# Kernel tuning notes

Measured on AMD Instinct MI355X. Metric: run time of the kernel, lower is better.

The kernel has to match this reference:

```python
import jax, jax.numpy as jnp
import numpy as np
import math

C = 128
N_HEAD = 4
GROUPS = 16
EPS = 1e-5


def group_norm(x, w, b):
    # x: [B, C, H, W], normalize per group over (C//G, H, W)
    B, Ch, H, W = x.shape
    xg = x.reshape(B, GROUPS, Ch // GROUPS, H, W)
    mu = xg.mean(axis=(2, 3, 4), keepdims=True)
    var = xg.var(axis=(2, 3, 4), keepdims=True)
    xn = (xg - mu) * jax.lax.rsqrt(var + EPS)
    xn = xn.reshape(B, Ch, H, W)
    return xn * w[None, :, None, None] + b[None, :, None, None]


def conv1x1(x, w, b=None):
    # w: [out, in]; x: [B, in, H, W]
    y = jnp.einsum('oc,bchw->bohw', w, x)
    if b is not None:
        y = y + b[None, :, None, None]
    return y


def cross_attn(q, k, v):
    # q, k, v: [B, C, H, W] -> split heads, flatten spatial
    B, Ch, H, W = q.shape
    d = Ch // N_HEAD
    L = H * W
    qh = q.reshape(B, N_HEAD, d, L)
    kh = k.reshape(B, N_HEAD, d, L)
    vh = v.reshape(B, N_HEAD, d, L)
    # scale by sqrt(channel) as in the original (not sqrt(head_dim))
    scores = jnp.einsum('bndq,bndk->bnqk', qh, kh) / math.sqrt(Ch)
    attn = jax.nn.softmax(scores, axis=-1)
    out = jnp.einsum('bnqk,bndk->bndq', attn, vh)
    return out.reshape(B, Ch, H, W)


def setup_inputs() -> dict:
    key = jax.random.key(0)
    ks = jax.random.split(key, 8)
    B, H, W = 2, 64, 64
    inp = {
        'x_A': jax.random.normal(ks[0], (B, C, H, W), jnp.float32),
        'x_B': jax.random.normal(ks[1], (B, C, H, W), jnp.float32),
        'gn_w_A': jnp.ones((C,), jnp.float32),
        'gn_b_A': jnp.zeros((C,), jnp.float32),
        'gn_w_B': jnp.ones((C,), jnp.float32),
        'gn_b_B': jnp.zeros((C,), jnp.float32),
        'w_qkv_A': jax.random.normal(ks[2], (3 * C, C), jnp.float32) / math.sqrt(C),
        'w_qkv_B': jax.random.normal(ks[3], (3 * C, C), jnp.float32) / math.sqrt(C),
        'w_out_A': jax.random.normal(ks[4], (C, C), jnp.float32) / math.sqrt(C),
        'b_out_A': jnp.zeros((C,), jnp.float32),
        'w_out_B': jax.random.normal(ks[5], (C, C), jnp.float32) / math.sqrt(C),
        'b_out_B': jnp.zeros((C,), jnp.float32),
    }
    return inp


def reference(x_A, x_B, gn_w_A, gn_b_A, gn_w_B, gn_b_B,
              w_qkv_A, w_qkv_B, w_out_A, b_out_A, w_out_B, b_out_B):
    xA = group_norm(x_A, gn_w_A, gn_b_A)
    xB = group_norm(x_B, gn_w_B, gn_b_B)
    qkvA = conv1x1(xA, w_qkv_A)  # [B, 3C, H, W]
    qkvB = conv1x1(xB, w_qkv_B)
    # torch view(b, n_head, head_dim*3, h, w).chunk(3, dim=2) splits within each head
    B, _, H, W = xA.shape
    d = C // N_HEAD
    qkvA = qkvA.reshape(B, N_HEAD, 3, d, H, W)
    qkvB = qkvB.reshape(B, N_HEAD, 3, d, H, W)
    qA, kA, vA = [qkvA[:, :, i].reshape(B, C, H, W) for i in range(3)]
    qB, kB, vB = [qkvB[:, :, i].reshape(B, C, H, W) for i in range(3)]
    # out_A: queries from B attend to keys/values of A; residual on normalized xA
    attn_out_A = cross_attn(qB, kA, vA)
    out_A = conv1x1(attn_out_A, w_out_A, b_out_A) + xA
    attn_out_B = cross_attn(qA, kB, vB)
    out_B = conv1x1(attn_out_B, w_out_B, b_out_B) + xB
    return (out_A, out_B)
```

## Files before the change

### kernel.cpp

```cpp
#include <hip/hip_runtime.h>
#include <hip/hip_bf16.h>

typedef __attribute__((ext_vector_type(8))) short short8;
typedef __attribute__((ext_vector_type(4))) short s16x4;
typedef __attribute__((ext_vector_type(4))) float f32x4;
typedef __attribute__((ext_vector_type(4))) float float4v;

#define L 4096
#define CCH 128
#define NH 4
#define HD 32
#define NSB 4
#define WQ_ELEMS 49152
#define WO_ELEMS 16384

static __device__ __forceinline__ unsigned short f2bf(float f) {
  unsigned int u = __float_as_uint(f);
  u += 0x7FFFu + ((u >> 16) & 1u);
  return (unsigned short)(u >> 16);
}

#if __has_builtin(__builtin_amdgcn_mfma_f32_16x16x16bf16_1k)
static __device__ __forceinline__ f32x4 mfma16(s16x4 a, s16x4 b, f32x4 c) {
  return __builtin_amdgcn_mfma_f32_16x16x16bf16_1k(a, b, c, 0, 0, 0);
}
#else
static __device__ __forceinline__ f32x4 mfma16(s16x4 a, s16x4 b, f32x4 c) {
  asm("v_mfma_f32_16x16x16_bf16 %0, %1, %2, %0"
      : "+v"(c) : "v"(a), "v"(b));
  return c;
}
#endif

__global__ void __launch_bounds__(256) wconv_kernel(
    const float* __restrict__ wqA, const float* __restrict__ wqB,
    const float* __restrict__ woA, const float* __restrict__ woB,
    unsigned short* __restrict__ wq, unsigned short* __restrict__ wo) {
  int i = (blockIdx.x * 256 + threadIdx.x) * 4;
  const float* src;
  unsigned short* dst;
  if (i < WQ_ELEMS)            { src = wqA + i;                     dst = wq + i; }
  else if (i < 2 * WQ_ELEMS)   { src = wqB + (i - WQ_ELEMS);        dst = wq + i; }
  else if (i < 2 * WQ_ELEMS + WO_ELEMS)
                               { src = woA + (i - 2 * WQ_ELEMS);    dst = wo + (i - 2 * WQ_ELEMS); }
  else                         { src = woB + (i - 2 * WQ_ELEMS - WO_ELEMS);
                                 dst = wo + (i - 2 * WQ_ELEMS); }
  float4v v = *(const float4v*)src;
  s16x4 o;
  #pragma unroll
  for (int j = 0; j < 4; ++j) o[j] = (short)f2bf(v[j]);
  *(s16x4*)dst = o;
}

__global__ void __launch_bounds__(256) gn_stats_kernel(
    const float* __restrict__ xA, const float* __restrict__ xB,
    float* __restrict__ stats) {
  int bid = blockIdx.x;
  int g = bid & 15;
  int b = (bid >> 4) & 1;
  int s = bid >> 5;
  const float* x = s ? xB : xA;
  const float* xb = x + (size_t)b * CCH * L + (size_t)g * 8 * L;
  int t = threadIdx.x;
  float sum = 0.f, sq = 0.f;
  for (int e = t * 4; e < 8 * L; e += 1024) {
    float4v v = *(const float4v*)(xb + e);
    #pragma unroll
    for (int j = 0; j < 4; ++j) { sum += v[j]; sq += v[j] * v[j]; }
  }
  #pragma unroll
  for (int off = 32; off; off >>= 1) {
    sum += __shfl_down(sum, off);
    sq  += __shfl_down(sq, off);
  }
  __shared__ float red[2][4];
  int w = t >> 6, lane = t & 63;
  if (lane == 0) { red[0][w] = sum; red[1][w] = sq; }
  __syncthreads();
  if (t == 0) {
    float S = red[0][0] + red[0][1] + red[0][2] + red[0][3];
    float Q = red[1][0] + red[1][1] + red[1][2] + red[1][3];
    float mu = S * (1.f / 32768.f);
    float var = Q * (1.f / 32768.f) - mu * mu;
    stats[bid * 2] = mu;
    stats[bid * 2 + 1] = rsqrtf(var + 1e-5f);
  }
}

__global__ void __launch_bounds__(256) gn_apply_kernel(
    const float* __restrict__ xA, const float* __restrict__ xB,
    const float* __restrict__ gwA, const float* __restrict__ gbA,
    const float* __restrict__ gwB, const float* __restrict__ gbB,
    const float* __restrict__ stats,
    float* __restrict__ xn, unsigned short* __restrict__ xnT) {
  int i = (blockIdx.x * 256 + threadIdx.x) * 8;
  int l = i & (L - 1);
  int c = (i >> 12) & 127;
  int sb = i >> 19;
  int s = sb >> 1, b = sb & 1, g = c >> 3;
  const float* x  = s ? xB : xA;
  const float* gw = s ? gwB : gwA;
  const float* gb = s ? gbB : gbA;
  float mu = stats[(sb * 16 + g) * 2];
  float rs = stats[(sb * 16 + g) * 2 + 1];
  float sc = rs * gw[c];
  float bi = gb[c] - mu * sc;
  const float* xp = x + (size_t)b * CCH * L + (size_t)c * L + l;
  float4v v0 = *(const float4v*)(xp);
  float4v v1 = *(const float4v*)(xp + 4);
  float r[8];
  #pragma unroll
  for (int j = 0; j < 4; ++j) { r[j] = v0[j] * sc + bi; r[4 + j] = v1[j] * sc + bi; }
  float* xo = xn + ((size_t)sb * CCH + c) * L + l;
  *(float4v*)(xo) = *(const float4v*)(r);
  *(float4v*)(xo + 4) = *(const float4v*)(r + 4);
  unsigned short* xt = xnT + ((size_t)sb * L + l) * CCH + c;
  #pragma unroll
  for (int j = 0; j < 8; ++j) xt[(size_t)j * CCH] = f2bf(r[j]);
}

__global__ void __launch_bounds__(256, 4) qkv_kernel(
    const unsigned short* __restrict__ wqbf,
    const unsigned short* __restrict__ xnT,
    unsigned short* __restrict__ qT, unsigned short* __restrict__ kT,
    unsigned short* __restrict__ vv) {
  int bid = blockIdx.x;
  int nc = bid & 63;
  int mt = (bid >> 6) % 24;
  int sb = bid / (24 * 64);
  int s = sb >> 1;
  const unsigned short* wq = wqbf + (size_t)s * WQ_ELEMS;
  int t = threadIdx.x;
  int w = t >> 6, lane = t & 63, ln = lane & 15, sub = lane >> 4;
  int obase = mt * 16;
  int lbase = nc * 64 + w * 16;
  const unsigned short* bbase = xnT + ((size_t)sb * L + lbase + ln) * CCH;
  const unsigned short* abase = wq + (size_t)(obase + ln) * CCH;
  f32x4 acc = {0.f, 0.f, 0.f, 0.f};
  #pragma unroll
  for (int kc = 0; kc < 4; ++kc) {
    int k0 = kc * 32 + sub * 8;
    short8 af = *(const short8*)(abase + k0);
    short8 bfr = *(const short8*)(bbase + k0);
    acc = __builtin_amdgcn_mfma_f32_16x16x32_bf16(af, bfr, acc, 0, 0, 0);
  }
  const float qscale = 0.08838834764831845f;
  int lcol = lbase + ln;
  #pragma unroll
  for (int r = 0; r < 4; ++r) {
    int o = obase + sub * 4 + r;
    int head = o / 96;
    int rem = o - head * 96;
    int part = rem >> 5;
    int dd = rem & 31;
    size_t bh = (size_t)sb * NH + head;
    if (part == 0)      qT[(bh * L + lcol) * HD + dd] = f2bf(acc[r] * qscale);
    else if (part == 1) kT[(bh * L + lcol) * HD + dd] = f2bf(acc[r]);
    else                vv[(bh * HD + dd) * L + lcol] = f2bf(acc[r]);
  }
}

__global__ void __launch_bounds__(256, 2) flash_kernel(
    const unsigned short* __restrict__ qT, const unsigned short* __restrict__ kT,
    const unsigned short* __restrict__ vv, unsigned short* __restrict__ ao) {
  int bid = blockIdx.x;
  int qt = bid & 31;
  int h  = (bid >> 5) & 3;
  int b  = (bid >> 7) & 1;
  int s  = bid >> 8;
  size_t bh_kv = (size_t)((s * 2 + b) * NH + h);
  size_t bh_q  = (size_t)(((s ^ 1) * 2 + b) * NH + h);
  const unsigned short* qTb = qT + bh_q * L * HD;
  const unsigned short* kTb = kT + bh_kv * L * HD;
  const unsigned short* vb  = vv + bh_kv * HD * L;

  int t = threadIdx.x;
  int w = t >> 6, lane = t & 63, ln = lane & 15, sub = lane >> 4;
  int qbase = qt * 128 + w * 32;

  short8 bq0 = *(const short8*)(qTb + (size_t)(qbase + ln) * HD + sub * 8);
  short8 bq1 = *(const short8*)(qTb + (size_t)(qbase + 16 + ln) * HD + sub * 8);

  f32x4 acc00 = {0.f, 0.f, 0.f, 0.f}, acc01 = {0.f, 0.f, 0.f, 0.f};
  f32x4 acc10 = {0.f, 0.f, 0.f, 0.f}, acc11 = {0.f, 0.f, 0.f, 0.f};
  float m0 = -1e30f, l0 = 0.f;
  float m1 = -1e30f, l1 = 0.f;

  for (int kt = 0; kt < L / 64; ++kt) {
    int kbase = kt * 64;
    short8 ak0 = *(const short8*)(kTb + (size_t)(kbase +  0 + ln) * HD + sub * 8);
    short8 ak1 = *(const short8*)(kTb + (size_t)(kbase + 16 + ln) * HD + sub * 8);
    short8 ak2 = *(const short8*)(kTb + (size_t)(kbase + 32 + ln) * HD + sub * 8);
    short8 ak3 = *(const short8*)(kTb + (size_t)(kbase + 48 + ln) * HD + sub * 8);
    s16x4 av00 = *(const s16x4*)(vb + (size_t)ln * L + kbase +  0 + sub * 4);
    s16x4 av01 = *(const s16x4*)(vb + (size_t)(16 + ln) * L + kbase +  0 + sub * 4);
    s16x4 av10 = *(const s16x4*)(vb + (size_t)ln * L + kbase + 16 + sub * 4);
    s16x4 av11 = *(const s16x4*)(vb + (size_t)(16 + ln) * L + kbase + 16 + sub * 4);
    s16x4 av20 = *(const s16x4*)(vb + (size_t)ln * L + kbase + 32 + sub * 4);
    s16x4 av21 = *(const s16x4*)(vb + (size_t)(16 + ln) * L + kbase + 32 + sub * 4);
    s16x4 av30 = *(const s16x4*)(vb + (size_t)ln * L + kbase + 48 + sub * 4);
    s16x4 av31 = *(const s16x4*)(vb + (size_t)(16 + ln) * L + kbase + 48 + sub * 4);

    f32x4 zz = {0.f, 0.f, 0.f, 0.f};
    f32x4 sa0 = __builtin_amdgcn_mfma_f32_16x16x32_bf16(ak0, bq0, zz, 0, 0, 0);
    f32x4 sa1 = __builtin_amdgcn_mfma_f32_16x16x32_bf16(ak1, bq0, zz, 0, 0, 0);
    f32x4 sa2 = __builtin_amdgcn_mfma_f32_16x16x32_bf16(ak2, bq0, zz, 0, 0, 0);
    f32x4 sa3 = __builtin_amdgcn_mfma_f32_16x16x32_bf16(ak3, bq0, zz, 0, 0, 0);
    f32x4 sb0 = __builtin_amdgcn_mfma_f32_16x16x32_bf16(ak0, bq1, zz, 0, 0, 0);
    f32x4 sb1 = __builtin_amdgcn_mfma_f32_16x16x32_bf16(ak1, bq1, zz, 0, 0, 0);
    f32x4 sb2 = __builtin_amdgcn_mfma_f32_16x16x32_bf16(ak2, bq1, zz, 0, 0, 0);
    f32x4 sb3 = __builtin_amdgcn_mfma_f32_16x16x32_bf16(ak3, bq1, zz, 0, 0, 0);

    s16x4 bp00, bp01, bp02, bp03;
    {
      float mx = fmaxf(fmaxf(sa0[0], sa0[1]), fmaxf(sa0[2], sa0[3]));
      mx = fmaxf(mx, fmaxf(fmaxf(sa1[0], sa1[1]), fmaxf(sa1[2], sa1[3])));
      mx = fmaxf(mx, fmaxf(fmaxf(sa2[0], sa2[1]), fmaxf(sa2[2], sa2[3])));
      mx = fmaxf(mx, fmaxf(fmaxf(sa3[0], sa3[1]), fmaxf(sa3[2], sa3[3])));
      mx = fmaxf(mx, __shfl_xor(mx, 16));
      mx = fmaxf(mx, __shfl_xor(mx, 32));
      float newm = fmaxf(m0, mx);
      float alpha = __expf(m0 - newm);
      float rsum = 0.f;
      #pragma unroll
      for (int r = 0; r < 4; ++r) {
        float p0 = __expf(sa0[r] - newm);
        float p1 = __expf(sa1[r] - newm);
        float p2 = __expf(sa2[r] - newm);
        float p3 = __expf(sa3[r] - newm);
        rsum += (p0 + p1) + (p2 + p3);
        bp00[r] = (short)f2bf(p0);
        bp01[r] = (short)f2bf(p1);
        bp02[r] = (short)f2bf(p2);
        bp03[r] = (short)f2bf(p3);
      }
      rsum += __shfl_xor(rsum, 16);
      rsum += __shfl_xor(rsum, 32);
      l0 = l0 * alpha + rsum;
      m0 = newm;
      #pragma unroll
      for (int r = 0; r < 4; ++r) { acc00[r] *= alpha; acc01[r] *= alpha; }
    }
    s16x4 bp10, bp11, bp12, bp13;
    {
      float mx = fmaxf(fmaxf(sb0[0], sb0[1]), fmaxf(sb0[2], sb0[3]));
      mx = fmaxf(mx, fmaxf(fmaxf(sb1[0], sb1[1]), fmaxf(sb1[2], sb1[3])));
      mx = fmaxf(mx, fmaxf(fmaxf(sb2[0], sb2[1]), fmaxf(sb2[2], sb2[3])));
      mx = fmaxf(mx, fmaxf(fmaxf(sb3[0], sb3[1]), fmaxf(sb3[2], sb3[3])));
      mx = fmaxf(mx, __shfl_xor(mx, 16));
      mx = fmaxf(mx, __shfl_xor(mx, 32));
      float newm = fmaxf(m1, mx);
      float alpha = __expf(m1 - newm);
      float rsum = 0.f;
      #pragma unroll
      for (int r = 0; r < 4; ++r) {
        float p0 = __expf(sb0[r] - newm);
        float p1 = __expf(sb1[r] - newm);
        float p2 = __expf(sb2[r] - newm);
        float p3 = __expf(sb3[r] - newm);
        rsum += (p0 + p1) + (p2 + p3);
        bp10[r] = (short)f2bf(p0);
        bp11[r] = (short)f2bf(p1);
        bp12[r] = (short)f2bf(p2);
        bp13[r] = (short)f2bf(p3);
      }
      rsum += __shfl_xor(rsum, 16);
      rsum += __shfl_xor(rsum, 32);
      l1 = l1 * alpha + rsum;
      m1 = newm;
      #pragma unroll
      for (int r = 0; r < 4; ++r) { acc10[r] *= alpha; acc11[r] *= alpha; }
    }
    acc00 = mfma16(av00, bp00, acc00); acc01 = mfma16(av01, bp00, acc01);
    acc00 = mfma16(av10, bp01, acc00); acc01 = mfma16(av11, bp01, acc01);
    acc00 = mfma16(av20, bp02, acc00); acc01 = mfma16(av21, bp02, acc01);
    acc00 = mfma16(av30, bp03, acc00); acc01 = mfma16(av31, bp03, acc01);
    acc10 = mfma16(av00, bp10, acc10); acc11 = mfma16(av01, bp10, acc11);
    acc10 = mfma16(av10, bp11, acc10); acc11 = mfma16(av11, bp11, acc11);
    acc10 = mfma16(av20, bp12, acc10); acc11 = mfma16(av21, bp12, acc11);
    acc10 = mfma16(av30, bp13, acc10); acc11 = mfma16(av31, bp13, acc11);
  }

  {
    float inv = 1.0f / l0;
    int qrow = qbase + ln;
    size_t rowoff = ((size_t)(s * 2 + b) * L + qrow) * CCH + h * HD;
    s16x4 o0, o1;
    #pragma unroll
    for (int r = 0; r < 4; ++r) {
      o0[r] = (short)f2bf(acc00[r] * inv);
      o1[r] = (short)f2bf(acc01[r] * inv);
    }
    *(s16x4*)(ao + rowoff + sub * 4) = o0;
    *(s16x4*)(ao + rowoff + 16 + sub * 4) = o1;
  }
  {
    float inv = 1.0f / l1;
    int qrow = qbase + 16 + ln;
    size_t rowoff = ((size_t)(s * 2 + b) * L + qrow) * CCH + h * HD;
    s16x4 o0, o1;
    #pragma unroll
    for (int r = 0; r < 4; ++r) {
      o0[r] = (short)f2bf(acc10[r] * inv);
      o1[r] = (short)f2bf(acc11[r] * inv);
    }
    *(s16x4*)(ao + rowoff + sub * 4) = o0;
    *(s16x4*)(ao + rowoff + 16 + sub * 4) = o1;
  }
}

__global__ void __launch_bounds__(256, 4) outproj_kernel(
    const unsigned short* __restrict__ wobf,
    const float* __restrict__ boA, const float* __restrict__ boB,
    const unsigned short* __restrict__ ao, const float* __restrict__ xn,
    float* __restrict__ out) {
  int bid = blockIdx.x;
  int nc = bid & 63;
  int mt = (bid >> 6) & 7;
  int sb = bid >> 9;
  int s = sb >> 1;
  int b = sb & 1;
  const unsigned short* wo = wobf + (size_t)s * WO_ELEMS;
  const float* bo = s ? boB : boA;
  int t = threadIdx.x;
  int w = t >> 6, lane = t & 63, ln = lane & 15, sub = lane >> 4;
  int obase = mt * 16;
  int lbase = nc * 64 + w * 16;
  const unsigned short* bbase = ao + ((size_t)sb * L + lbase + ln) * CCH;
  const unsigned short* abase = wo + (size_t)(obase + ln) * CCH;
  f32x4 acc = {0.f, 0.f, 0.f, 0.f};
  #pragma unroll
  for (int kc = 0; kc < 4; ++kc) {
    int k0 = kc * 32 + sub * 8;
    short8 af = *(const short8*)(abase + k0);
    short8 bfr = *(const short8*)(bbase + k0);
    acc = __builtin_amdgcn_mfma_f32_16x16x32_bf16(af, bfr, acc, 0, 0, 0);
  }
  int lcol = lbase + ln;
  #pragma unroll
  for (int r = 0; r < 4; ++r) {
    int o = obase + sub * 4 + r;
    out[(size_t)s * (2 * CCH * L) + ((size_t)b * CCH + o) * L + lcol] =
        acc[r] + bo[o] + xn[((size_t)sb * CCH + o) * L + lcol];
  }
}

extern "C" void kernel_launch(void* const* d_in, const int* in_sizes, int n_in,
                              void* d_out, int out_size, void* d_ws, size_t ws_size,
                              hipStream_t stream) {
  (void)in_sizes; (void)n_in; (void)out_size; (void)ws_size;
  const float* xA  = (const float*)d_in[0];
  const float* xB  = (const float*)d_in[1];
  const float* gwA = (const float*)d_in[2];
  const float* gbA = (const float*)d_in[3];
  const float* gwB = (const float*)d_in[4];
  const float* gbB = (const float*)d_in[5];
  const float* wqA = (const float*)d_in[6];
  const float* wqB = (const float*)d_in[7];
  const float* woA = (const float*)d_in[8];
  const float* boA = (const float*)d_in[9];
  const float* woB = (const float*)d_in[10];
  const float* boB = (const float*)d_in[11];
  float* out = (float*)d_out;

  char* ws = (char*)d_ws;
  size_t off = 0;
  float* xn = (float*)(ws + off);            off += (size_t)NSB * CCH * L * sizeof(float);
  unsigned short* xnT = (unsigned short*)(ws + off); off += (size_t)NSB * L * CCH * 2;
  unsigned short* qT  = (unsigned short*)(ws + off); off += (size_t)NSB * NH * L * HD * 2;
  unsigned short* kT  = (unsigned short*)(ws + off); off += (size_t)NSB * NH * L * HD * 2;
  unsigned short* vv  = (unsigned short*)(ws + off); off += (size_t)NSB * NH * HD * L * 2;
  unsigned short* ao  = (unsigned short*)(ws + off); off += (size_t)NSB * L * CCH * 2;
  float* stats = (float*)(ws + off);         off += 64 * 2 * sizeof(float);
  unsigned short* wqbf = (unsigned short*)(ws + off); off += (size_t)2 * WQ_ELEMS * 2;
  unsigned short* wobf = (unsigned short*)(ws + off); off += (size_t)2 * WO_ELEMS * 2;

  wconv_kernel<<<dim3(128), dim3(256), 0, stream>>>(wqA, wqB, woA, woB, wqbf, wobf);
  gn_stats_kernel<<<dim3(64), dim3(256), 0, stream>>>(xA, xB, stats);
  gn_apply_kernel<<<dim3(1024), dim3(256), 0, stream>>>(xA, xB, gwA, gbA, gwB, gbB,
                                                        stats, xn, xnT);
  qkv_kernel<<<dim3(NSB * 24 * 64), dim3(256), 0, stream>>>(wqbf, xnT, qT, kT, vv);
  flash_kernel<<<dim3(512), dim3(256), 0, stream>>>(qT, kT, vv, ao);
  outproj_kernel<<<dim3(NSB * 8 * 64), dim3(256), 0, stream>>>(wobf, boA, boB, ao, xn, out);
}
```

Baseline: 287.7 us.

## Stage K/V tiles through double-buffered LDS and remap block order in flash kernel

Each flash block previously had every wave load its own K and V fragments straight from global memory. Now the block loads each 64-key K/V tile once, cooperatively, into a double-buffered LDS area in MFMA fragment order. The global load for the next tile is issued before computing on the current one, so load latency overlaps compute. Block IDs are also permuted so consecutive blocks map to different heads and batches, which spreads L2 use. The cost is one __syncthreads per tile, extra LDS traffic and 16 KB of LDS per block, which may limit occupancy.

```diff
diff --git a/kernel.cpp b/kernel.cpp
--- a/kernel.cpp
+++ b/kernel.cpp
@@ -163,7 +163,8 @@
 __global__ void __launch_bounds__(256, 2) flash_kernel(
     const unsigned short* __restrict__ qT, const unsigned short* __restrict__ kT,
     const unsigned short* __restrict__ vv, unsigned short* __restrict__ ao) {
-  int bid = blockIdx.x;
+  int bid0 = blockIdx.x;
+  int bid = (bid0 & 7) * 64 + (bid0 >> 3);
   int qt = bid & 31;
   int h  = (bid >> 5) & 3;
   int b  = (bid >> 7) & 1;
@@ -178,29 +179,49 @@
   int w = t >> 6, lane = t & 63, ln = lane & 15, sub = lane >> 4;
   int qbase = qt * 128 + w * 32;
 
+  __shared__ unsigned short lds_k[2][2048];
+  __shared__ unsigned short lds_v[2][2048];
+
+  const unsigned short* gK = kTb + (size_t)(w * 16 + (lane >> 2)) * HD + (lane & 3) * 8;
+  int dstK = ((w * 4 + (lane & 3)) * 16 + (lane >> 2)) * 8;
+  int dV = w * 8 + (lane >> 3);
+  const unsigned short* gV = vb + (size_t)dV * L + (lane & 7) * 8;
+  int ttv = (lane & 7) >> 1, halfv = w >> 1, lnv = (w & 1) * 8 + (lane >> 3);
+  int sub0 = ((lane & 7) & 1) * 2;
+  int dstV0 = (((ttv * 2 + halfv) * 4 + sub0) * 16 + lnv) * 4;
+
   short8 bq0 = *(const short8*)(qTb + (size_t)(qbase + ln) * HD + sub * 8);
   short8 bq1 = *(const short8*)(qTb + (size_t)(qbase + 16 + ln) * HD + sub * 8);
+
+  {
+    short8 sk = *(const short8*)(gK);
+    short8 sv = *(const short8*)(gV);
+    s16x4 svlo, svhi;
+    #pragma unroll
+    for (int j = 0; j < 4; ++j) { svlo[j] = sv[j]; svhi[j] = sv[4 + j]; }
+    *(short8*)&lds_k[0][dstK] = sk;
+    *(s16x4*)&lds_v[0][dstV0] = svlo;
+    *(s16x4*)&lds_v[0][dstV0 + 64] = svhi;
+  }
+  __syncthreads();
 
   f32x4 acc00 = {0.f, 0.f, 0.f, 0.f}, acc01 = {0.f, 0.f, 0.f, 0.f};
   f32x4 acc10 = {0.f, 0.f, 0.f, 0.f}, acc11 = {0.f, 0.f, 0.f, 0.f};
   float m0 = -1e30f, l0 = 0.f;
   float m1 = -1e30f, l1 = 0.f;
 
-  for (int kt = 0; kt < L / 64; ++kt) {
-    int kbase = kt * 64;
-    short8 ak0 = *(const short8*)(kTb + (size_t)(kbase +  0 + ln) * HD + sub * 8);
-    short8 ak1 = *(const short8*)(kTb + (size_t)(kbase + 16 + ln) * HD + sub * 8);
-    short8 ak2 = *(const short8*)(kTb + (size_t)(kbase + 32 + ln) * HD + sub * 8);
-    short8 ak3 = *(const short8*)(kTb + (size_t)(kbase + 48 + ln) * HD + sub * 8);
-    s16x4 av00 = *(const s16x4*)(vb + (size_t)ln * L + kbase +  0 + sub * 4);
-    s16x4 av01 = *(const s16x4*)(vb + (size_t)(16 + ln) * L + kbase +  0 + sub * 4);
-    s16x4 av10 = *(const s16x4*)(vb + (size_t)ln * L + kbase + 16 + sub * 4);
-    s16x4 av11 = *(const s16x4*)(vb + (size_t)(16 + ln) * L + kbase + 16 + sub * 4);
-    s16x4 av20 = *(const s16x4*)(vb + (size_t)ln * L + kbase + 32 + sub * 4);
-    s16x4 av21 = *(const s16x4*)(vb + (size_t)(16 + ln) * L + kbase + 32 + sub * 4);
-    s16x4 av30 = *(const s16x4*)(vb + (size_t)ln * L + kbase + 48 + sub * 4);
-    s16x4 av31 = *(const s16x4*)(vb + (size_t)(16 + ln) * L + kbase + 48 + sub * 4);
-
+  const int NT = L / 64;
+  for (int kt = 0; kt < NT; ++kt) {
+    int cur = kt & 1;
+    int nk = (kt + 1 < NT) ? kt + 1 : kt;
+    short8 sk = *(const short8*)(gK + (size_t)nk * 2048);
+    short8 sv = *(const short8*)(gV + nk * 64);
+    __builtin_amdgcn_sched_barrier(0);
+
+    short8 ak0 = *(const short8*)&lds_k[cur][((0 * 4 + sub) * 16 + ln) * 8];
+    short8 ak1 = *(const short8*)&lds_k[cur][((1 * 4 + sub) * 16 + ln) * 8];
+    short8 ak2 = *(const short8*)&lds_k[cur][((2 * 4 + sub) * 16 + ln) * 8];
+    short8 ak3 = *(const short8*)&lds_k[cur][((3 * 4 + sub) * 16 + ln) * 8];
     f32x4 zz = {0.f, 0.f, 0.f, 0.f};
     f32x4 sa0 = __builtin_amdgcn_mfma_f32_16x16x32_bf16(ak0, bq0, zz, 0, 0, 0);
     f32x4 sa1 = __builtin_amdgcn_mfma_f32_16x16x32_bf16(ak1, bq0, zz, 0, 0, 0);
@@ -271,14 +292,25 @@
       #pragma unroll
       for (int r = 0; r < 4; ++r) { acc10[r] *= alpha; acc11[r] *= alpha; }
     }
-    acc00 = mfma16(av00, bp00, acc00); acc01 = mfma16(av01, bp00, acc01);
-    acc00 = mfma16(av10, bp01, acc00); acc01 = mfma16(av11, bp01, acc01);
-    acc00 = mfma16(av20, bp02, acc00); acc01 = mfma16(av21, bp02, acc01);
-    acc00 = mfma16(av30, bp03, acc00); acc01 = mfma16(av31, bp03, acc01);
-    acc10 = mfma16(av00, bp10, acc10); acc11 = mfma16(av01, bp10, acc11);
-    acc10 = mfma16(av10, bp11, acc10); acc11 = mfma16(av11, bp11, acc11);
-    acc10 = mfma16(av20, bp12, acc10); acc11 = mfma16(av21, bp12, acc11);
-    acc10 = mfma16(av30, bp13, acc10); acc11 = mfma16(av31, bp13, acc11);
+    #pragma unroll
+    for (int tt = 0; tt < 4; ++tt) {
+      s16x4 av0 = *(const s16x4*)&lds_v[cur][(((tt * 2 + 0) * 4 + sub) * 16 + ln) * 4];
+      s16x4 av1 = *(const s16x4*)&lds_v[cur][(((tt * 2 + 1) * 4 + sub) * 16 + ln) * 4];
+      s16x4 bpa = (tt == 0) ? bp00 : (tt == 1) ? bp01 : (tt == 2) ? bp02 : bp03;
+      s16x4 bpb = (tt == 0) ? bp10 : (tt == 1) ? bp11 : (tt == 2) ? bp12 : bp13;
+      acc00 = mfma16(av0, bpa, acc00); acc01 = mfma16(av1, bpa, acc01);
+      acc10 = mfma16(av0, bpb, acc10); acc11 = mfma16(av1, bpb, acc11);
+    }
+
+    {
+      s16x4 svlo, svhi;
+      #pragma unroll
+      for (int j = 0; j < 4; ++j) { svlo[j] = sv[j]; svhi[j] = sv[4 + j]; }
+      *(short8*)&lds_k[cur ^ 1][dstK] = sk;
+      *(s16x4*)&lds_v[cur ^ 1][dstV0] = svlo;
+      *(s16x4*)&lds_v[cur ^ 1][dstV0 + 64] = svhi;
+    }
+    __syncthreads();
   }
 
   {
```

New measurement: 245.1 us. 1.17x faster.
